# Kernel tuning notes

Measured on AMD Instinct MI355X. Metric: run time of the kernel, lower is better.

## Reference

```python
import jax, jax.numpy as jnp
import numpy as np

NUM_EMBEDDINGS = 1024
EMBEDDING_DIM = 128
COMMITMENT_COST = 0.25
B, T = 32, 2048


def setup_inputs() -> dict:
    key = jax.random.key(0)
    k1, k2 = jax.random.split(key)
    inputs = jax.random.normal(k1, (B, T, EMBEDDING_DIM), dtype=jnp.float32)
    lim = 1.0 / NUM_EMBEDDINGS
    embedding_weight = jax.random.uniform(
        k2, (NUM_EMBEDDINGS, EMBEDDING_DIM), dtype=jnp.float32,
        minval=-lim, maxval=lim)
    return {"inputs": inputs, "embedding_weight": embedding_weight}


def reference(inputs, embedding_weight):
    D = embedding_weight.shape[1]
    flat = inputs.reshape(-1, D)                                  # [N, D]
    # squared L2 distances to every codebook entry: [N, K]
    distances = (
        jnp.sum(flat * flat, axis=1, keepdims=True)
        + jnp.sum(embedding_weight * embedding_weight, axis=1)
        - 2.0 * jnp.matmul(flat, embedding_weight.T)
    )
    encoding_indices = jnp.argmin(distances, axis=1)              # [N]
    quantized = embedding_weight[encoding_indices].reshape(inputs.shape)
    sg = jax.lax.stop_gradient
    e_latent_loss = jnp.mean((sg(quantized) - inputs) ** 2)
    q_latent_loss = jnp.mean((quantized - sg(inputs)) ** 2)
    loss = q_latent_loss + COMMITMENT_COST * e_latent_loss
    # straight-through estimator
    quantized = inputs + sg(quantized - inputs)
    return (loss, quantized, encoding_indices)
```

## Files before the change

### kernel.cpp

```cpp
#include <hip/hip_runtime.h>

#define NROWS 65536
#define KC    1024
#define DIM   128
#define W_DIST 5e-5f

typedef short  bf16x8 __attribute__((ext_vector_type(8)));
typedef float  f32x4  __attribute__((ext_vector_type(4)));
typedef float  f32x16 __attribute__((ext_vector_type(16)));

#define ZERO16 ((f32x16){0.f,0.f,0.f,0.f,0.f,0.f,0.f,0.f,0.f,0.f,0.f,0.f,0.f,0.f,0.f,0.f})

__device__ __forceinline__ unsigned short f2bf_rne(float f) {
    unsigned int u = __float_as_uint(f);
    u += 0x7FFFu + ((u >> 16) & 1u);
    return (unsigned short)(u >> 16);
}
__device__ __forceinline__ float bf2f(unsigned short h) {
    return __uint_as_float(((unsigned int)h) << 16);
}

__device__ __forceinline__ void gll16(const unsigned short* g, short* l) {
    __builtin_amdgcn_global_load_lds(
        (const __attribute__((address_space(1))) unsigned int*)g,
        (__attribute__((address_space(3))) unsigned int*)l,
        16, 0, 0);
}

template <int N>
__device__ __forceinline__ void vmwait() {
    if constexpr (N == 8)      asm volatile("s_waitcnt vmcnt(8)" ::: "memory");
    else if constexpr (N == 4) asm volatile("s_waitcnt vmcnt(4)" ::: "memory");
    else if constexpr (N == 2) asm volatile("s_waitcnt vmcnt(2)" ::: "memory");
    else                       asm volatile("s_waitcnt vmcnt(0)" ::: "memory");
}

__device__ __forceinline__ float np_sumsq_128(const float* v) {
    float r[8];
    #pragma unroll
    for (int j = 0; j < 8; ++j) r[j] = __fmul_rn(v[j], v[j]);
    #pragma unroll
    for (int i = 1; i < 16; ++i)
        #pragma unroll
        for (int j = 0; j < 8; ++j)
            r[j] = __fadd_rn(r[j], __fmul_rn(v[i * 8 + j], v[i * 8 + j]));
    return __fadd_rn(__fadd_rn(__fadd_rn(r[0], r[1]), __fadd_rn(r[2], r[3])),
                     __fadd_rn(__fadd_rn(r[4], r[5]), __fadd_rn(r[6], r[7])));
}

__global__ __launch_bounds__(256) void vq_prep(const float* __restrict__ emb,
        float* __restrict__ enorm,
        unsigned short* __restrict__ eh, unsigned short* __restrict__ em) {
    const int k = blockIdx.x * 256 + threadIdx.x;
    if (k >= KC) return;
    float v[DIM];
    const float4* e = reinterpret_cast<const float4*>(emb + (size_t)k * DIM);
    #pragma unroll
    for (int i = 0; i < 32; ++i) {
        float4 t = e[i];
        v[i * 4 + 0] = t.x; v[i * 4 + 1] = t.y;
        v[i * 4 + 2] = t.z; v[i * 4 + 3] = t.w;
    }
    enorm[k] = np_sumsq_128(v);
    unsigned short* ph = eh + (size_t)k * DIM;
    unsigned short* pm = em + (size_t)k * DIM;
    #pragma unroll
    for (int i = 0; i < 16; ++i) {
        unsigned int h[8], m[8];
        #pragma unroll
        for (int j = 0; j < 8; ++j) {
            float f = v[i * 8 + j];
            unsigned short hh = f2bf_rne(f);
            h[j] = hh;
            m[j] = f2bf_rne(f - bf2f(hh));
        }
        uint4 vh = {h[0] | (h[1] << 16), h[2] | (h[3] << 16),
                    h[4] | (h[5] << 16), h[6] | (h[7] << 16)};
        uint4 vm = {m[0] | (m[1] << 16), m[2] | (m[3] << 16),
                    m[4] | (m[5] << 16), m[6] | (m[7] << 16)};
        *reinterpret_cast<uint4*>(ph + i * 8) = vh;
        *reinterpret_cast<uint4*>(pm + i * 8) = vm;
    }
}

__global__ __launch_bounds__(256, 2) void vq_mfma(
        const float* __restrict__ x,
        const unsigned short* __restrict__ eh, const unsigned short* __restrict__ em,
        const float* __restrict__ enorm,
        int* __restrict__ bestk, float* __restrict__ idx_out,
        int* __restrict__ fb_cnt, int* __restrict__ fb_rows) {
    const int tid  = threadIdx.x;
    const int lane = tid & 63;
    const int wid  = tid >> 6;
    const int lr31 = lane & 31;
    const int hi   = lane >> 5;
    const int rtile = blockIdx.x * 128 + wid * 32;

    __shared__ short ldsE[3][2][4096];
    __shared__ float s_enorm[KC];

    const int u0 = wid * 128 + lane;
    const int u1 = wid * 128 + 64 + lane;
    const int src0 = (u0 & 31) * DIM + (u0 >> 5) * 8;
    const int src1 = (u1 & 31) * DIM + (u1 >> 5) * 8;
    const int dst0 = wid * 128 * 8;
    const int dst1 = (wid * 128 + 64) * 8;

#define VQ_STAGE(T, B)                                                      \
    do {                                                                    \
        const unsigned short* _gh = eh + (size_t)(T) * 4096;                \
        const unsigned short* _gm = em + (size_t)(T) * 4096;                \
        gll16(_gh + src0, &ldsE[B][0][dst0]);                               \
        gll16(_gh + src1, &ldsE[B][0][dst1]);                               \
        gll16(_gm + src0, &ldsE[B][1][dst0]);                               \
        gll16(_gm + src1, &ldsE[B][1][dst1]);                               \
    } while (0)

    bf16x8 fxh[8], fxm[8];
    {
        const float* px = x + (size_t)(rtile + lr31) * DIM + hi * 8;
        #pragma unroll
        for (int s = 0; s < 8; ++s) {
            float4 a = *reinterpret_cast<const float4*>(px + s * 16);
            float4 b = *reinterpret_cast<const float4*>(px + s * 16 + 4);
            float f[8] = {a.x, a.y, a.z, a.w, b.x, b.y, b.z, b.w};
            bf16x8 vh, vm;
            #pragma unroll
            for (int j = 0; j < 8; ++j) {
                unsigned short hh = f2bf_rne(f[j]);
                vh[j] = (short)hh;
                vm[j] = (short)f2bf_rne(f[j] - bf2f(hh));
            }
            fxh[s] = vh; fxm[s] = vm;
        }
    }
    #pragma unroll
    for (int s = 0; s < 8; ++s)
        asm volatile("" : "+v"(fxh[s]), "+v"(fxm[s]));

    *reinterpret_cast<float4*>(&s_enorm[tid * 4]) =
        *reinterpret_cast<const float4*>(&enorm[tid * 4]);

    VQ_STAGE(0, 0);
    VQ_STAGE(1, 1);

    asm volatile("s_waitcnt lgkmcnt(0)" ::: "memory");
    __builtin_amdgcn_s_barrier();

    float m1 = 1e30f, m2 = 1e30f; int k1 = 0;
    f32x16 aE, dE, aO, dO;

#define VQ_EPI(T, PA, PD)                                                   \
    do {                                                                    \
        const int _kb = (T) * 32 + (hi << 2);                               \
        _Pragma("unroll")                                                   \
        for (int g = 0; g < 4; ++g) {                                       \
            const f32x4 _nr = *reinterpret_cast<const f32x4*>(&s_enorm[_kb + g * 8]); \
            _Pragma("unroll")                                               \
            for (int j = 0; j < 4; ++j) {                                   \
                const int _r = g * 4 + j;                                   \
                float _v = fmaf(-2.0f, PA[_r] + PD[_r], _nr[j]);            \
                int _kk = _kb + g * 8 + j;                                  \
                bool _lt = _v < m1;                                         \
                m2 = fminf(m2, fmaxf(m1, _v));                              \
                k1 = _lt ? _kk : k1;                                        \
                m1 = fminf(m1, _v);                                         \
            }                                                               \
        }                                                                   \
    } while (0)

#define VQ_ITER(T, B, SB, CA, CD, PA, PD, VMN, DOSTAGE, DOEPI)              \
    do {                                                                    \
        vmwait<VMN>();                                                      \
        __builtin_amdgcn_s_barrier();                                       \
        asm volatile("" ::: "memory");                                      \
        CA = ZERO16; CD = ZERO16;                                           \
        __builtin_amdgcn_s_setprio(1);                                      \
        _Pragma("unroll")                                                   \
        for (int s = 0; s < 8; ++s) {                                       \
            const int _u = ((s * 2 + hi) * 32 + lr31) * 8;                  \
            bf16x8 feh = *reinterpret_cast<const bf16x8*>(&ldsE[B][0][_u]); \
            bf16x8 fem = *reinterpret_cast<const bf16x8*>(&ldsE[B][1][_u]); \
            CA = __builtin_amdgcn_mfma_f32_32x32x16_bf16(feh, fxh[s], CA, 0, 0, 0); \
            CD = __builtin_amdgcn_mfma_f32_32x32x16_bf16(feh, fxm[s], CD, 0, 0, 0); \
            CD = __builtin_amdgcn_mfma_f32_32x32x16_bf16(fem, fxh[s], CD, 0, 0, 0); \
        }                                                                   \
        __builtin_amdgcn_s_setprio(0);                                      \
        if (DOSTAGE) { VQ_STAGE((T) + 2, SB); }                             \
        if (DOEPI)   { VQ_EPI((T) - 1, PA, PD); }                           \
    } while (0)

    VQ_ITER(0, 0, 2, aE, dE, aO, dO, 4, 1, 0);
    VQ_ITER(1, 1, 0, aO, dO, aE, dE, 4, 1, 1);
    VQ_ITER(2, 2, 1, aE, dE, aO, dO, 4, 1, 1);
    VQ_ITER(3, 0, 2, aO, dO, aE, dE, 4, 1, 1);
    VQ_ITER(4, 1, 0, aE, dE, aO, dO, 4, 1, 1);
    VQ_ITER(5, 2, 1, aO, dO, aE, dE, 4, 1, 1);
    for (int tb = 6; tb < 30; tb += 6) {
        VQ_ITER(tb + 0, 0, 2, aE, dE, aO, dO, 4, 1, 1);
        VQ_ITER(tb + 1, 1, 0, aO, dO, aE, dE, 4, 1, 1);
        VQ_ITER(tb + 2, 2, 1, aE, dE, aO, dO, 4, 1, 1);
        VQ_ITER(tb + 3, 0, 2, aO, dO, aE, dE, 4, 1, 1);
        VQ_ITER(tb + 4, 1, 0, aE, dE, aO, dO, 4, 1, 1);
        VQ_ITER(tb + 5, 2, 1, aO, dO, aE, dE, 4, 1, 1);
    }
    VQ_ITER(30, 0, 2, aE, dE, aO, dO, 4, 0, 1);
    VQ_ITER(31, 1, 0, aO, dO, aE, dE, 0, 0, 1);
    VQ_EPI(31, aO, dO);
#undef VQ_ITER
#undef VQ_EPI
#undef VQ_STAGE

    {
        float om1 = __shfl_xor(m1, 32, 64);
        float om2 = __shfl_xor(m2, 32, 64);
        int   ok1 = __shfl_xor(k1, 32, 64);
        float mx = fmaxf(m1, om1);
        m2 = fminf(fminf(m2, om2), mx);
        bool take = (om1 < m1) || (om1 == m1 && ok1 < k1);
        k1 = take ? ok1 : k1;
        m1 = fminf(m1, om1);
    }
    if (lane < 32) {
        const int row = rtile + lane;
        if (m2 - m1 < W_DIST) {
            int slot = atomicAdd(fb_cnt, 1);
            fb_rows[slot] = row;
        } else {
            bestk[row] = k1;
            idx_out[row] = (float)k1;
        }
    }
}

__global__ __launch_bounds__(512) void vq_fallback(
        const float* __restrict__ x, const float* __restrict__ emb,
        const float* __restrict__ enorm,
        const int* __restrict__ fb_cnt, const int* __restrict__ fb_rows,
        int* __restrict__ bestk, float* __restrict__ idx_out) {
    const int tid  = threadIdx.x;
    const int lane = tid & 63;
    const int wid  = tid >> 6;
    const int nb = *fb_cnt;

    __shared__ float sx[8][DIM];
    __shared__ float s_xn[8];
    __shared__ float swv[8][8];
    __shared__ int   swk[8][8];

    const float en0 = enorm[tid];
    const float en1 = enorm[tid + 512];
    const float4* e0p = reinterpret_cast<const float4*>(emb + (size_t)tid * DIM);
    const float4* e1p = reinterpret_cast<const float4*>(emb + (size_t)(tid + 512) * DIM);

    for (int base = blockIdx.x * 8; base < nb; base += gridDim.x * 8) {
        const int R = min(8, nb - base);
        {
            const int r = tid >> 6;
            const int c2 = (tid & 63) * 2;
            const int slot = fb_rows[min(base + r, nb - 1)];
            float2 v = *reinterpret_cast<const float2*>(x + (size_t)slot * DIM + c2);
            sx[r][c2] = v.x; sx[r][c2 + 1] = v.y;
        }
        __syncthreads();
        if (tid < 8) s_xn[tid] = np_sumsq_128(&sx[tid][0]);
        __syncthreads();

        float a0[8][4], a1[8][4];
        #pragma unroll
        for (int r = 0; r < 8; ++r)
            #pragma unroll
            for (int c = 0; c < 4; ++c) { a0[r][c] = 0.f; a1[r][c] = 0.f; }

        for (int q = 0; q < 32; q += 4) {
            float4 e0v[4], e1v[4];
            #pragma unroll
            for (int j = 0; j < 4; ++j) { e0v[j] = e0p[q + j]; e1v[j] = e1p[q + j]; }
            #pragma unroll
            for (int j = 0; j < 4; ++j) {
                #pragma unroll
                for (int r = 0; r < 8; ++r) {
                    float4 xv = *reinterpret_cast<const float4*>(&sx[r][(q + j) * 4]);
                    a0[r][0] = fmaf(xv.x, e0v[j].x, a0[r][0]);
                    a0[r][1] = fmaf(xv.y, e0v[j].y, a0[r][1]);
                    a0[r][2] = fmaf(xv.z, e0v[j].z, a0[r][2]);
                    a0[r][3] = fmaf(xv.w, e0v[j].w, a0[r][3]);
                    a1[r][0] = fmaf(xv.x, e1v[j].x, a1[r][0]);
                    a1[r][1] = fmaf(xv.y, e1v[j].y, a1[r][1]);
                    a1[r][2] = fmaf(xv.z, e1v[j].z, a1[r][2]);
                    a1[r][3] = fmaf(xv.w, e1v[j].w, a1[r][3]);
                }
            }
        }

        float cv[8]; int ck[8];
        #pragma unroll
        for (int r = 0; r < 8; ++r) {
            float xn = s_xn[r];
            float d0 = __fadd_rn(__fadd_rn(a0[r][0], a0[r][1]),
                                 __fadd_rn(a0[r][2], a0[r][3]));
            float s0 = __fsub_rn(__fadd_rn(xn, en0), __fmul_rn(2.0f, d0));
            float d1 = __fadd_rn(__fadd_rn(a1[r][0], a1[r][1]),
                                 __fadd_rn(a1[r][2], a1[r][3]));
            float s1 = __fsub_rn(__fadd_rn(xn, en1), __fmul_rn(2.0f, d1));
            bool t1 = (s1 < s0);
            cv[r] = t1 ? s1 : s0;
            ck[r] = t1 ? tid + 512 : tid;
        }
        #pragma unroll
        for (int off = 1; off < 64; off <<= 1) {
            #pragma unroll
            for (int r = 0; r < 8; ++r) {
                float ov = __shfl_xor(cv[r], off, 64);
                int   ok = __shfl_xor(ck[r], off, 64);
                bool take = (ov < cv[r]) || (ov == cv[r] && ok < ck[r]);
                cv[r] = take ? ov : cv[r];
                ck[r] = take ? ok : ck[r];
            }
        }
        if (lane == 0) {
            #pragma unroll
            for (int r = 0; r < 8; ++r) { swv[wid][r] = cv[r]; swk[wid][r] = ck[r]; }
        }
        __syncthreads();
        if (tid < R) {
            float bv = swv[0][tid]; int bk = swk[0][tid];
            #pragma unroll
            for (int w = 1; w < 8; ++w) {
                float v = swv[w][tid]; int k = swk[w][tid];
                bool take = (v < bv) || (v == bv && k < bk);
                bv = take ? v : bv;
                bk = take ? k : bk;
            }
            const int row = fb_rows[base + tid];
            bestk[row] = bk;
            idx_out[row] = (float)bk;
        }
        __syncthreads();
    }
}

__global__ __launch_bounds__(256) void vq_gather(
        const float* __restrict__ x, const float* __restrict__ emb,
        const int* __restrict__ bestk, float* __restrict__ quant,
        double* __restrict__ partials) {
    const int t = blockIdx.x * 256 + threadIdx.x;
    const int r = t >> 4;
    const int c = (t & 15) * 8;
    const int bk = bestk[r];
    const float4* ep = reinterpret_cast<const float4*>(emb + (size_t)bk * DIM + c);
    const float4* xp = reinterpret_cast<const float4*>(x + (size_t)r * DIM + c);
    float4 e0 = ep[0], e1 = ep[1];
    float4 x0 = xp[0], x1 = xp[1];
    float* q = quant + (size_t)r * DIM + c;
    q[0] = e0.x; q[1] = e0.y; q[2] = e0.z; q[3] = e0.w;
    q[4] = e1.x; q[5] = e1.y; q[6] = e1.z; q[7] = e1.w;
    float d0 = e0.x - x0.x, d1 = e0.y - x0.y, d2 = e0.z - x0.z, d3 = e0.w - x0.w;
    float d4 = e1.x - x1.x, d5 = e1.y - x1.y, d6 = e1.z - x1.z, d7 = e1.w - x1.w;
    float acc = fmaf(d0, d0, fmaf(d1, d1, fmaf(d2, d2, d3 * d3)))
              + fmaf(d4, d4, fmaf(d5, d5, fmaf(d6, d6, d7 * d7)));
    #pragma unroll
    for (int off = 32; off > 0; off >>= 1) acc += __shfl_down(acc, off, 64);

    __shared__ float sacc[4];
    if ((threadIdx.x & 63) == 0) sacc[threadIdx.x >> 6] = acc;
    __syncthreads();
    if (threadIdx.x == 0)
        partials[blockIdx.x] =
            (double)sacc[0] + (double)sacc[1] + (double)sacc[2] + (double)sacc[3];
}

__global__ __launch_bounds__(256) void vq_loss(
        const double* __restrict__ partials, float* __restrict__ out) {
    double s = 0.0;
    #pragma unroll
    for (int i = 0; i < 16; ++i) s += partials[threadIdx.x + i * 256];
    #pragma unroll
    for (int off = 32; off > 0; off >>= 1) s += __shfl_down(s, off, 64);
    __shared__ double sd[4];
    if ((threadIdx.x & 63) == 0) sd[threadIdx.x >> 6] = s;
    __syncthreads();
    if (threadIdx.x == 0)
        out[0] = (float)((sd[0] + sd[1] + sd[2] + sd[3]) * (1.25 / 8388608.0));
}

extern "C" void kernel_launch(void* const* d_in, const int* in_sizes, int n_in,
                              void* d_out, int out_size, void* d_ws, size_t ws_size,
                              hipStream_t stream) {
    const float* x   = (const float*)d_in[0];
    const float* emb = (const float*)d_in[1];

    float* out      = (float*)d_out;
    float* loss_out = out;
    float* quant    = out + 1;
    float* idx_out  = out + 1 + (size_t)NROWS * DIM;

    char* ws = (char*)d_ws;
    int*    fb_cnt   = (int*)(ws + 8);
    float*  enorm    = (float*)(ws + 1024);
    int*    fb_rows  = (int*)(ws + 16384);
    int*    bestk    = (int*)(ws + 278528);
    unsigned short* eh = (unsigned short*)(ws + 557056);
    unsigned short* em = (unsigned short*)(ws + 819200);
    double* partials = (double*)(ws + 1081344);

    hipMemsetAsync(ws, 0, 16, stream);
    vq_prep<<<4, 256, 0, stream>>>(emb, enorm, eh, em);
    vq_mfma<<<512, 256, 0, stream>>>(x, eh, em, enorm,
                                     bestk, idx_out, fb_cnt, fb_rows);
    vq_fallback<<<1024, 512, 0, stream>>>(x, emb, enorm, fb_cnt, fb_rows,
                                          bestk, idx_out);
    vq_gather<<<4096, 256, 0, stream>>>(x, emb, bestk, quant, partials);
    vq_loss<<<1, 256, 0, stream>>>(partials, loss_out);
}
```

Baseline: 109.5 us.

## Process codebook tiles in pairs with one barrier per two tiles

Replaces the triple-buffered one-tile-per-barrier pipeline with a four-buffer scheme that handles two 32-entry codebook tiles per barrier and prefetches the next pair. This halves the number of workgroup barriers and vmcnt waits in the main loop. In exchange it grows LDS use (four buffers instead of three), which may reduce occupancy. It also waits on vmcnt(0), so the prefetch has only about one pair of MFMA work in which to hide its latency.

```diff
diff --git a/kernel.cpp b/kernel.cpp
--- a/kernel.cpp
+++ b/kernel.cpp
@@ -25,14 +25,6 @@
         (const __attribute__((address_space(1))) unsigned int*)g,
         (__attribute__((address_space(3))) unsigned int*)l,
         16, 0, 0);
-}
-
-template <int N>
-__device__ __forceinline__ void vmwait() {
-    if constexpr (N == 8)      asm volatile("s_waitcnt vmcnt(8)" ::: "memory");
-    else if constexpr (N == 4) asm volatile("s_waitcnt vmcnt(4)" ::: "memory");
-    else if constexpr (N == 2) asm volatile("s_waitcnt vmcnt(2)" ::: "memory");
-    else                       asm volatile("s_waitcnt vmcnt(0)" ::: "memory");
 }
 
 __device__ __forceinline__ float np_sumsq_128(const float* v) {
@@ -96,7 +88,7 @@
     const int hi   = lane >> 5;
     const int rtile = blockIdx.x * 128 + wid * 32;
 
-    __shared__ short ldsE[3][2][4096];
+    __shared__ short ldsE[4][2][4096];
     __shared__ float s_enorm[KC];
 
     const int u0 = wid * 128 + lane;
@@ -169,12 +161,8 @@
         }                                                                   \
     } while (0)
 
-#define VQ_ITER(T, B, SB, CA, CD, PA, PD, VMN, DOSTAGE, DOEPI)              \
+#define VQ_MFMA24(B, CA, CD)                                                \
     do {                                                                    \
-        vmwait<VMN>();                                                      \
-        __builtin_amdgcn_s_barrier();                                       \
-        asm volatile("" ::: "memory");                                      \
-        CA = ZERO16; CD = ZERO16;                                           \
         __builtin_amdgcn_s_setprio(1);                                      \
         _Pragma("unroll")                                                   \
         for (int s = 0; s < 8; ++s) {                                       \
@@ -186,28 +174,26 @@
             CD = __builtin_amdgcn_mfma_f32_32x32x16_bf16(fem, fxh[s], CD, 0, 0, 0); \
         }                                                                   \
         __builtin_amdgcn_s_setprio(0);                                      \
-        if (DOSTAGE) { VQ_STAGE((T) + 2, SB); }                             \
-        if (DOEPI)   { VQ_EPI((T) - 1, PA, PD); }                           \
     } while (0)
 
-    VQ_ITER(0, 0, 2, aE, dE, aO, dO, 4, 1, 0);
-    VQ_ITER(1, 1, 0, aO, dO, aE, dE, 4, 1, 1);
-    VQ_ITER(2, 2, 1, aE, dE, aO, dO, 4, 1, 1);
-    VQ_ITER(3, 0, 2, aO, dO, aE, dE, 4, 1, 1);
-    VQ_ITER(4, 1, 0, aE, dE, aO, dO, 4, 1, 1);
-    VQ_ITER(5, 2, 1, aO, dO, aE, dE, 4, 1, 1);
-    for (int tb = 6; tb < 30; tb += 6) {
-        VQ_ITER(tb + 0, 0, 2, aE, dE, aO, dO, 4, 1, 1);
-        VQ_ITER(tb + 1, 1, 0, aO, dO, aE, dE, 4, 1, 1);
-        VQ_ITER(tb + 2, 2, 1, aE, dE, aO, dO, 4, 1, 1);
-        VQ_ITER(tb + 3, 0, 2, aO, dO, aE, dE, 4, 1, 1);
-        VQ_ITER(tb + 4, 1, 0, aE, dE, aO, dO, 4, 1, 1);
-        VQ_ITER(tb + 5, 2, 1, aO, dO, aE, dE, 4, 1, 1);
-    }
-    VQ_ITER(30, 0, 2, aE, dE, aO, dO, 4, 0, 1);
-    VQ_ITER(31, 1, 0, aO, dO, aE, dE, 0, 0, 1);
+    for (int S = 0; S < 16; ++S) {
+        asm volatile("s_waitcnt vmcnt(0)" ::: "memory");
+        __builtin_amdgcn_s_barrier();
+        asm volatile("" ::: "memory");
+        const int b0 = (S & 1) * 2;
+        aE = ZERO16; dE = ZERO16;
+        VQ_MFMA24(b0, aE, dE);
+        if (S < 15) {
+            VQ_STAGE(2 * S + 2, b0 ^ 2);
+            VQ_STAGE(2 * S + 3, (b0 ^ 2) + 1);
+        }
+        if (S > 0) VQ_EPI(2 * S - 1, aO, dO);
+        aO = ZERO16; dO = ZERO16;
+        VQ_MFMA24(b0 + 1, aO, dO);
+        VQ_EPI(2 * S, aE, dE);
+    }
     VQ_EPI(31, aO, dO);
-#undef VQ_ITER
+#undef VQ_MFMA24
 #undef VQ_EPI
 #undef VQ_STAGE
 
```

New measurement: 112.3 us. 1.03x slower.
